# Kernel optimization log

Hardware: AMD Instinct MI355X
Metric: run time of the kernel (lower is better)

Reference implementation:

```python
import jax, jax.numpy as jnp
import numpy as np

N = 50000      # nodes
E = 800000     # edges (before self-loops)
F_IN = 256     # feature_size
H = 96         # hidden_channels
G = 64         # graphs in batch
NC = 4         # num_classes
EPS = 1e-5     # BatchNorm eps


def _lrelu(x, s=0.01):
    return jnp.where(x >= 0, x, s * x)


def _gat(x, W, a_s, a_d, b, src, dst):
    # PyG GATConv, heads=1: linear transform, edge-wise LeakyReLU(0.2) scores,
    # segment softmax over destination nodes, scatter-add aggregation.
    h = x @ W                                                  # [N,H]
    e = _lrelu((h * a_s).sum(-1)[src] + (h * a_d).sum(-1)[dst], 0.2)  # [E+N]
    m = jax.ops.segment_max(e, dst, num_segments=N)
    ee = jnp.exp(e - m[dst])
    denom = jax.ops.segment_sum(ee, dst, num_segments=N)
    alpha = ee / denom[dst]
    return jax.ops.segment_sum(alpha[:, None] * h[src], dst, num_segments=N) + b


def _bn(x, g, b):
    # training-mode BatchNorm over the node dimension
    mu = x.mean(0)
    var = ((x - mu) ** 2).mean(0)
    return g * (x - mu) / jnp.sqrt(var + EPS) + b


def setup_inputs() -> dict:
    key = jax.random.key(0)
    ks = jax.random.split(key, 20)
    p = lambda i, sh: jax.random.normal(ks[i], sh, jnp.float32) * 0.05
    inp = {
        "x": jax.random.normal(ks[0], (N, F_IN), jnp.float32),
        "edge_index": jax.random.randint(ks[1], (2, E), 0, N),
        "batch": jnp.sort(jax.random.randint(ks[2], (N,), 0, G)),
        "embed_W": p(3, (F_IN, H)), "embed_b": jnp.zeros((H,), jnp.float32),
        "conv1_W": p(4, (H, H)), "conv1_as": p(5, (H,)), "conv1_ad": p(6, (H,)), "conv1_b": jnp.zeros((H,), jnp.float32),
        "conv2_W": p(7, (H, H)), "conv2_as": p(8, (H,)), "conv2_ad": p(9, (H,)), "conv2_b": jnp.zeros((H,), jnp.float32),
        "conv3_W": p(10, (H, H)), "conv3_as": p(11, (H,)), "conv3_ad": p(12, (H,)), "conv3_b": jnp.zeros((H,), jnp.float32),
        "fc1_W": p(13, (H, H)), "fc1_b": jnp.zeros((H,), jnp.float32),
        "fc2_W": p(14, (H, H)), "fc2_b": jnp.zeros((H,), jnp.float32),
        "bn1_g": jnp.ones((H,), jnp.float32), "bn1_b": jnp.zeros((H,), jnp.float32),
        "bn2_g": jnp.ones((H,), jnp.float32), "bn2_b": jnp.zeros((H,), jnp.float32),
        "bn3_g": jnp.ones((H,), jnp.float32), "bn3_b": jnp.zeros((H,), jnp.float32),
        "fc3_W": p(15, (H, H // 2)), "fc3_b": jnp.zeros((H // 2,), jnp.float32),
        "fc4_W": p(16, (H // 2, NC)), "fc4_b": jnp.zeros((NC,), jnp.float32),
    }
    return inp


def reference(x, edge_index, batch, embed_W, embed_b,
              conv1_W, conv1_as, conv1_ad, conv1_b,
              conv2_W, conv2_as, conv2_ad, conv2_b,
              conv3_W, conv3_as, conv3_ad, conv3_b,
              fc1_W, fc1_b, fc2_W, fc2_b,
              bn1_g, bn1_b, bn2_g, bn2_b, bn3_g, bn3_b,
              fc3_W, fc3_b, fc4_W, fc4_b):
    loops = jnp.arange(N)
    src = jnp.concatenate([edge_index[0], loops])   # GATConv add_self_loops=True
    dst = jnp.concatenate([edge_index[1], loops])

    h = _lrelu(x @ embed_W + embed_b)
    identity = h
    h = _lrelu(_bn(_gat(h, conv1_W, conv1_as, conv1_ad, conv1_b, src, dst), bn1_g, bn1_b)) + identity
    h = _lrelu(h @ fc1_W + fc1_b)
    h = _lrelu(_bn(_gat(h, conv2_W, conv2_as, conv2_ad, conv2_b, src, dst), bn2_g, bn2_b)) + identity
    h = _lrelu(h @ fc2_W + fc2_b)
    h = _lrelu(_bn(_gat(h, conv3_W, conv3_as, conv3_ad, conv3_b, src, dst), bn3_g, bn3_b)) + identity

    # Poincare ball expmap0 with c=1: tanh(||u||) * u / ||u||
    n = jnp.maximum(jnp.linalg.norm(h, axis=-1, keepdims=True), 1e-15)
    h = jnp.tanh(n) * h / n

    cnt = jax.ops.segment_sum(jnp.ones((N,), h.dtype), batch, num_segments=G)
    pooled = jax.ops.segment_sum(h, batch, num_segments=G) / jnp.maximum(cnt, 1.0)[:, None]

    o = _lrelu(pooled @ fc3_W + fc3_b)
    return o @ fc4_W + fc4_b
```

## Files before the change

### kernel.cpp

```cpp
#include <hip/hip_runtime.h>
#include <hip/hip_bf16.h>

#define DEVINL __device__ __forceinline__

constexpr int N_NODES = 50000;
constexpr int N_EDGES = 800000;
constexpr int F_IN    = 256;
constexpr int H       = 96;
constexpr int NG      = 64;
constexpr float BN_EPS = 1e-5f;
constexpr int SLOT    = 64;
constexpr int NREP    = 8;
constexpr int REPSZ   = NG * H + NG;
constexpr int EPB     = 8;
constexpr int ECHUNK  = 256 * EPB;

typedef short bf16x8 __attribute__((ext_vector_type(8)));
typedef float f32x4  __attribute__((ext_vector_type(4)));

DEVINL float bf2f(unsigned int u) {
    union { unsigned int i; float f; } c; c.i = u << 16; return c.f;
}
DEVINL unsigned short f2bf(float f) {
    union { float f; unsigned int i; } c; c.f = f;
    unsigned int x = c.i;
    return (unsigned short)((x + 0x7fffu + ((x >> 16) & 1u)) >> 16);
}
DEVINL float lrelu01(float v) { return v >= 0.f ? v : 0.01f * v; }
DEVINL float ldf(const void* p, size_t i, int f32) {
    return f32 ? ((const float*)p)[i] : bf2f(((const unsigned short*)p)[i]);
}

__global__ __launch_bounds__(256) void detect_fill_k(const unsigned short* __restrict__ x,
                                                     int* __restrict__ flag,
                                                     int* __restrict__ fill)
{
    if (blockIdx.x == 0 && threadIdx.x < 64) {
        int l = threadIdx.x;
        float f = bf2f(x[l]);
        bool huge = !(fabsf(f) <= 1e4f);
        unsigned long long m = __ballot(huge);
        if (l == 0) flag[0] = (__popcll(m) >= 8) ? 1 : 0;
    }
    int i = blockIdx.x * 256 + threadIdx.x;
    if (i < N_NODES) fill[i] = 0;
}

__global__ __launch_bounds__(256) void wpackall_k(
    const void* __restrict__ sE, const void* __restrict__ s0,
    const void* __restrict__ s1, const void* __restrict__ s2,
    const void* __restrict__ s3, const void* __restrict__ s4,
    const int* __restrict__ dflag,
    unsigned short* __restrict__ dE, unsigned short* __restrict__ d0,
    unsigned short* __restrict__ d1, unsigned short* __restrict__ d2,
    unsigned short* __restrict__ d3, unsigned short* __restrict__ d4)
{
    int b = blockIdx.x;
    const void* src; unsigned short* dst; int K, i0;
    if (b < 96) { src = sE; dst = dE; K = F_IN; i0 = b * 256; }
    else {
        int m = (b - 96) / 36, r = (b - 96) % 36;
        K = H; i0 = r * 256;
        if      (m == 0) { src = s0; dst = d0; }
        else if (m == 1) { src = s1; dst = d1; }
        else if (m == 2) { src = s2; dst = d2; }
        else if (m == 3) { src = s3; dst = d3; }
        else             { src = s4; dst = d4; }
    }
    int i = i0 + threadIdx.x;
    if (i >= K * 96) return;
    int c   = i / 3072;
    int rem = i - c * 3072;
    int t    = rem >> 9;
    int rem2 = rem & 511;
    int l = rem2 >> 3, j = rem2 & 7;
    int k = c * 32 + (l >> 4) * 8 + j;
    int n = t * 16 + (l & 15);
    if (dflag[0]) dst[i] = f2bf(((const float*)src)[k * 96 + n]);
    else          dst[i] = ((const unsigned short*)src)[k * 96 + n];
}

template<int EPI, int AWS, int SD, int ABN, int SCAT, int K>
__global__ __launch_bounds__(256) void mgemm_k(
    const void* __restrict__ Ap, const unsigned short* __restrict__ Wpk,
    const void* __restrict__ bp, const int* __restrict__ dflag,
    unsigned short* __restrict__ out, unsigned short* __restrict__ out2,
    const void* __restrict__ as_, const void* __restrict__ ad_,
    float* __restrict__ s, float* __restrict__ d,
    const float* __restrict__ coefp, const unsigned short* __restrict__ idn,
    const int* __restrict__ ei, int* __restrict__ fill,
    unsigned short* __restrict__ colw, int e0, int e1, int ngb,
    int M)
{
    constexpr int NCH = K / 32;
    __shared__ unsigned short Wlds[K * 96];

    if (SCAT && (int)blockIdx.x >= ngb) {
        int b0 = e0 + ((int)blockIdx.x - ngb) * ECHUNK + (int)threadIdx.x;
        int sv[EPB], dv[EPB];
        bool ok[EPB];
        #pragma unroll
        for (int j = 0; j < EPB; j++) {
            int e = b0 + j * 256;
            ok[j] = (e < e1);
            int ee = ok[j] ? e : e0;
            sv[j] = ei[ee];
            dv[j] = ei[N_EDGES + ee];
        }
        int p[EPB];
        #pragma unroll
        for (int j = 0; j < EPB; j++)
            p[j] = ok[j] ? atomicAdd(&fill[dv[j]], 1) : SLOT;
        #pragma unroll
        for (int j = 0; j < EPB; j++)
            if (p[j] < SLOT) colw[(size_t)dv[j] * SLOT + p[j]] = (unsigned short)sv[j];
        return;
    }

    {
        const uint4* ws = (const uint4*)Wpk;
        uint4* wd = (uint4*)Wlds;
        #pragma unroll 4
        for (int i = threadIdx.x; i < K * 12; i += 256) wd[i] = ws[i];
    }
    __syncthreads();

    const int f32  = AWS ? 0 : dflag[0];
    const int wf32 = dflag[0];
    const int l    = threadIdx.x & 63;
    const int wave = threadIdx.x >> 6;
    const int row0 = blockIdx.x * 64 + wave * 16;
    const int m    = l & 15;
    const int q    = l >> 4;
    const int arow = row0 + m;
    const bool aok = arow < M;

    bf16x8 av[NCH];
    #pragma unroll
    for (int c = 0; c < NCH; c++) {
        bf16x8 a = {};
        if (aok) {
            if (ABN) {
                const int f0 = c * 32 + q * 8;
                uint4 xu = *(const uint4*)((const unsigned short*)Ap + (size_t)arow * K + f0);
                uint4 iu = *(const uint4*)(idn + (size_t)arow * K + f0);
                unsigned int xs[4] = { xu.x, xu.y, xu.z, xu.w };
                unsigned int is[4] = { iu.x, iu.y, iu.z, iu.w };
                #pragma unroll
                for (int jj = 0; jj < 4; jj++) {
                    int f = f0 + 2 * jj;
                    float v0 = lrelu01(bf2f(xs[jj] & 0xffff) * coefp[f]     + coefp[96 + f])     + bf2f(is[jj] & 0xffff);
                    float v1 = lrelu01(bf2f(xs[jj] >> 16)    * coefp[f + 1] + coefp[96 + f + 1]) + bf2f(is[jj] >> 16);
                    a[2 * jj]     = (short)f2bf(v0);
                    a[2 * jj + 1] = (short)f2bf(v1);
                }
            } else if (f32) {
                const float* A = (const float*)Ap + (size_t)arow * K + c * 32 + q * 8;
                #pragma unroll
                for (int j = 0; j < 8; j++) a[j] = (short)f2bf(A[j]);
            } else {
                a = *(const bf16x8*)((const unsigned short*)Ap + (size_t)arow * K + c * 32 + q * 8);
            }
        }
        av[c] = a;
    }

    f32x4 acc[6] = {};
    const bf16x8* wl = (const bf16x8*)Wlds;
    #pragma unroll
    for (int c = 0; c < NCH; c++) {
        const int base = c * 384 + l;
        #pragma unroll
        for (int t = 0; t < 6; t++)
            acc[t] = __builtin_amdgcn_mfma_f32_16x16x32_bf16(av[c], wl[base + t * 64], acc[t], 0, 0, 0);
    }

    float bv[6];
    if (EPI > 0) {
        #pragma unroll
        for (int t = 0; t < 6; t++) bv[t] = ldf(bp, t * 16 + m, wf32);
    }
    #pragma unroll
    for (int r = 0; r < 4; r++) {
        int rr = row0 + q * 4 + r;
        if (rr >= M) continue;
        size_t o = (size_t)rr * 96 + m;
        #pragma unroll
        for (int t = 0; t < 6; t++) {
            float v = acc[t][r];
            if (EPI > 0) v = lrelu01(v + bv[t]);
            unsigned short sv = f2bf(v);
            out[o + t * 16] = sv;
            if (EPI == 2) out2[o + t * 16] = sv;
        }
    }

    if (SD) {
        float asv[6], adv[6];
        #pragma unroll
        for (int t = 0; t < 6; t++) {
            asv[t] = ldf(as_, t * 16 + m, wf32);
            adv[t] = ldf(ad_, t * 16 + m, wf32);
        }
        #pragma unroll
        for (int r = 0; r < 4; r++) {
            float ps = 0.f, pd = 0.f;
            #pragma unroll
            for (int t = 0; t < 6; t++) {
                ps = fmaf(acc[t][r], asv[t], ps);
                pd = fmaf(acc[t][r], adv[t], pd);
            }
            #pragma unroll
            for (int off = 1; off < 16; off <<= 1) {
                ps += __shfl_xor(ps, off);
                pd += __shfl_xor(pd, off);
            }
            int rr = row0 + q * 4 + r;
            if (m == 0 && rr < M) { s[rr] = ps; d[rr] = pd; }
        }
    }
}

__global__ __launch_bounds__(256) void agg_k(
    const unsigned short* __restrict__ h2, const float* __restrict__ s,
    const float* __restrict__ d, const int* __restrict__ fill,
    const unsigned short* __restrict__ col, const void* __restrict__ bias,
    const int* __restrict__ dflag, unsigned short* __restrict__ out,
    float* __restrict__ bnsum, float* __restrict__ zp, int M)
{
    __shared__ uint2 uwb[4][80];
    if (blockIdx.x == 0 && threadIdx.x < 192) bnsum[threadIdx.x] = 0.f;
    if (zp) {
        int zi = blockIdx.x * 256 + threadIdx.x;
        if (zi < NREP * REPSZ) zp[zi] = 0.f;
    }
    int f32 = dflag[0];
    int v = (blockIdx.x * blockDim.x + threadIdx.x) >> 6;
    int l = threadIdx.x & 63;
    int wv = threadIdx.x >> 6;
    if (v >= M) return;
    int st   = v * SLOT;
    int degr = min(fill[v], SLOT - 1);
    int deg  = degr + 1;

    float dv = d[v];
    int u = 0; float e = -1e30f;
    if (l < degr) {
        u = col[st + l];
        float t = s[u] + dv;
        e = t >= 0.f ? t : 0.2f * t;
    } else if (l == degr) {
        u = v;
        float t = s[v] + dv;
        e = t >= 0.f ? t : 0.2f * t;
    }
    float lm = e;
    #pragma unroll
    for (int off = 32; off > 0; off >>= 1) lm = fmaxf(lm, __shfl_xor(lm, off));
    float w = (l < deg) ? __expf(e - lm) : 0.f;
    float ls = w;
    #pragma unroll
    for (int off = 32; off > 0; off >>= 1) ls += __shfl_xor(ls, off);
    float rden = 1.0f / ls;

    uwb[wv][l] = make_uint2((unsigned int)u, __float_as_uint(w));
    if (l < 16) uwb[wv][64 + l] = make_uint2(0u, 0u);

    bool hw = (l < 48);
    int  c2 = 2 * l;
    float a0 = 0.f, a1 = 0.f;
    const uint2* myuw = uwb[wv];
    for (int j = 0; j < deg; j += 16) {
        uint2 p[16];
        #pragma unroll
        for (int k = 0; k < 16; k++) p[k] = myuw[j + k];
        if (hw) {
            unsigned int hv[16];
            #pragma unroll
            for (int k = 0; k < 16; k++)
                hv[k] = *(const unsigned int*)(h2 + (size_t)p[k].x * 96 + c2);
            #pragma unroll
            for (int k = 0; k < 16; k++) {
                float wj = __uint_as_float(p[k].y);
                a0 = fmaf(wj, bf2f(hv[k] & 0xffff), a0);
                a1 = fmaf(wj, bf2f(hv[k] >> 16),    a1);
            }
        }
    }
    if (hw) {
        float b0 = ldf(bias, c2,     f32);
        float b1 = ldf(bias, c2 + 1, f32);
        unsigned int o = (unsigned int)f2bf(a0 * rden + b0)
                       | ((unsigned int)f2bf(a1 * rden + b1) << 16);
        *(unsigned int*)(out + (size_t)v * 96 + c2) = o;
    }
}

__global__ __launch_bounds__(192) void bnstats_k(const unsigned short* __restrict__ x,
                                                 float* __restrict__ sums, int M)
{
    int c  = threadIdx.x % 96;
    int g2 = threadIdx.x / 96;
    float s = 0.f, q = 0.f;
    for (int r = blockIdx.x * 2 + g2; r < M; r += gridDim.x * 2) {
        float v = bf2f(x[(size_t)r * 96 + c]);
        s += v; q += v * v;
    }
    __shared__ float lsd[192], lqd[192];
    lsd[threadIdx.x] = s; lqd[threadIdx.x] = q;
    __syncthreads();
    if (g2 == 0) {
        atomicAdd(&sums[c],      s + lsd[threadIdx.x + 96]);
        atomicAdd(&sums[96 + c], q + lqd[threadIdx.x + 96]);
    }
}

__global__ void bncoef_k(const float* __restrict__ sums,
                         const void* __restrict__ g_,
                         const void* __restrict__ b_,
                         const int* __restrict__ dflag,
                         float* __restrict__ coef)
{
    int c = threadIdx.x;
    if (c >= 96) return;
    int f32 = dflag[0];
    float mu  = sums[c] * (1.f / N_NODES);
    float var = sums[96 + c] * (1.f / N_NODES) - mu * mu;
    float rinv = 1.0f / sqrtf(var + BN_EPS);
    float sc = ldf(g_, c, f32) * rinv;
    coef[c]      = sc;
    coef[96 + c] = ldf(b_, c, f32) - mu * sc;
}

__global__ __launch_bounds__(256) void bnpool_k(
    const unsigned short* __restrict__ h, const float* __restrict__ coef,
    const unsigned short* __restrict__ iden, const int* __restrict__ batch,
    float* __restrict__ pooled8, int M)
{
    int w = (blockIdx.x * blockDim.x + threadIdx.x) >> 6;
    int l = threadIdx.x & 63;
    int v0 = w * 16;
    if (v0 >= M) return;
    float* P = pooled8 + (blockIdx.x & (NREP - 1)) * REPSZ;
    float* C = P + NG * H;
    bool hw = (l < 48);
    int  c2 = 2 * l;
    float sc0 = 0.f, sc1 = 0.f, sh0 = 0.f, sh1 = 0.f;
    if (hw) {
        sc0 = coef[c2]; sc1 = coef[c2 + 1];
        sh0 = coef[96 + c2]; sh1 = coef[97 + c2];
    }
    int nv = min(16, M - v0);

    int gb[16];
    #pragma unroll
    for (int k = 0; k < 16; k++) gb[k] = batch[v0 + min(k, nv - 1)];

    float x0[16], x1[16], q[16];
    #pragma unroll
    for (int k = 0; k < 16; k++) { x0[k] = 0.f; x1[k] = 0.f; q[k] = 0.f; }
    if (hw) {
        unsigned int xu[16], iu[16];
        #pragma unroll
        for (int k = 0; k < 16; k++) {
            int v = v0 + k;
            if (k < nv) {
                xu[k] = *(const unsigned int*)(h    + (size_t)v * 96 + c2);
                iu[k] = *(const unsigned int*)(iden + (size_t)v * 96 + c2);
            } else { xu[k] = 0u; iu[k] = 0u; }
        }
        #pragma unroll
        for (int k = 0; k < 16; k++) {
            x0[k] = lrelu01(bf2f(xu[k] & 0xffff) * sc0 + sh0) + bf2f(iu[k] & 0xffff);
            x1[k] = lrelu01(bf2f(xu[k] >> 16)    * sc1 + sh1) + bf2f(iu[k] >> 16);
            q[k]  = x0[k] * x0[k] + x1[k] * x1[k];
        }
    }

    #pragma unroll
    for (int off = 32; off > 0; off >>= 1) {
        #pragma unroll
        for (int k = 0; k < 16; k++) q[k] += __shfl_xor(q[k], off);
    }

    float f[16];
    #pragma unroll
    for (int k = 0; k < 16; k++) {
        float n = fmaxf(sqrtf(q[k]), 1e-15f);
        if (n < 15.f) {
            float t = __expf(2.f * n);
            f[k] = (t - 1.f) / ((t + 1.f) * n);
        } else {
            f[k] = 1.f / n;
        }
    }

    float a0 = 0.f, a1 = 0.f, cnt = 0.f;
    int curg = -1;
    for (int k = 0; k < nv; k++) {
        int g = gb[k];
        if (g != curg) {
            if (curg >= 0) {
                if (hw) {
                    atomicAdd(&P[curg * 96 + c2],     a0);
                    atomicAdd(&P[curg * 96 + c2 + 1], a1);
                }
                if (l == 0) atomicAdd(&C[curg], cnt);
            }
            a0 = a1 = 0.f; cnt = 0.f; curg = g;
        }
        a0 = fmaf(f[k], x0[k], a0);
        a1 = fmaf(f[k], x1[k], a1);
        cnt += 1.f;
    }
    if (curg >= 0) {
        if (hw) {
            atomicAdd(&P[curg * 96 + c2],     a0);
            atomicAdd(&P[curg * 96 + c2 + 1], a1);
        }
        if (l == 0) atomicAdd(&C[curg], cnt);
    }
}

__global__ __launch_bounds__(64) void head_k(const float* __restrict__ pooled8,
                                             const void* __restrict__ w3,
                                             const void* __restrict__ b3,
                                             const void* __restrict__ w4,
                                             const void* __restrict__ b4,
                                             const int* __restrict__ dflag,
                                             void* __restrict__ outv)
{
    int g = blockIdx.x;
    int t = threadIdx.x;
    int f32 = dflag[0];
    __shared__ float p[96];
    __shared__ float o[48];
    float cs = 0.f;
    #pragma unroll
    for (int r = 0; r < NREP; r++) cs += pooled8[r * REPSZ + NG * H + g];
    float inv = 1.0f / fmaxf(cs, 1.0f);
    for (int c = t; c < 96; c += 64) {
        float v = 0.f;
        #pragma unroll
        for (int r = 0; r < NREP; r++) v += pooled8[r * REPSZ + g * 96 + c];
        p[c] = v * inv;
    }
    __syncthreads();
    if (t < 48) {
        float a = ldf(b3, t, f32);
        #pragma unroll
        for (int c = 0; c < 96; c++) a = fmaf(p[c], ldf(w3, (size_t)c * 48 + t, f32), a);
        o[t] = lrelu01(a);
    }
    __syncthreads();
    if (t < 4) {
        float a = ldf(b4, t, f32);
        #pragma unroll
        for (int j = 0; j < 48; j++) a = fmaf(o[j], ldf(w4, j * 4 + t, f32), a);
        if (f32) ((float*)outv)[g * 4 + t] = a;
        else     ((unsigned short*)outv)[g * 4 + t] = f2bf(a);
    }
}

extern "C" void kernel_launch(void* const* d_in, const int* in_sizes, int n_in,
                              void* d_out, int out_size, void* d_ws, size_t ws_size,
                              hipStream_t stream)
{
    const void* x     = d_in[0];
    const int*  ei    = (const int*)d_in[1];
    const int*  batch = (const int*)d_in[2];
    const void* embW  = d_in[3];
    const void* embB  = d_in[4];
    const void* convW[3]  = { d_in[5],  d_in[9],  d_in[13] };
    const void* convAs[3] = { d_in[6],  d_in[10], d_in[14] };
    const void* convAd[3] = { d_in[7],  d_in[11], d_in[15] };
    const void* convB[3]  = { d_in[8],  d_in[12], d_in[16] };
    const void* fcW[2]    = { d_in[17], d_in[19] };
    const void* fcB[2]    = { d_in[18], d_in[20] };
    const void* bnG[3]    = { d_in[21], d_in[23], d_in[25] };
    const void* bnB[3]    = { d_in[22], d_in[24], d_in[26] };
    const void* fc3W = d_in[27];
    const void* fc3b = d_in[28];
    const void* fc4W = d_in[29];
    const void* fc4b = d_in[30];

    char* wp_ = (char*)d_ws;
    auto alloc = [&](size_t b) { char* p = wp_; wp_ += (b + 255) & ~(size_t)255; return p; };
    int*   dflag = (int*)alloc(256);
    unsigned short* ident = (unsigned short*)alloc((size_t)N_NODES * H * 2);
    unsigned short* hA    = (unsigned short*)alloc((size_t)N_NODES * H * 2);
    unsigned short* hB    = (unsigned short*)alloc((size_t)N_NODES * H * 2);
    float* s_sc  = (float*)alloc((size_t)N_NODES * 4);
    float* d_sc  = (float*)alloc((size_t)N_NODES * 4);
    float* bnsum = (float*)alloc(192 * 4);
    float* coef  = (float*)alloc(192 * 4);
    float* pooled8 = (float*)alloc((size_t)NREP * REPSZ * 4);
    int*   fill  = (int*)alloc((size_t)N_NODES * 4);
    unsigned short* col = (unsigned short*)alloc((size_t)N_NODES * SLOT * 2);
    unsigned short* wpkEmb = (unsigned short*)alloc((size_t)F_IN * 96 * 2);
    unsigned short* wpkS[5];
    for (int i = 0; i < 5; i++) wpkS[i] = (unsigned short*)alloc((size_t)H * 96 * 2);

    const int GM = (N_NODES + 63) / 64;
    const int GW = (N_NODES * 64 + 255) / 256;
    const int GP = ((N_NODES + 15) / 16 * 64 + 255) / 256;
    const int GF = (N_NODES + 255) / 256;
    const int EH = N_EDGES / 2;
    const int GS = (EH + ECHUNK - 1) / ECHUNK;

    detect_fill_k<<<GF, 256, 0, stream>>>((const unsigned short*)x, dflag, fill);

    wpackall_k<<<276, 256, 0, stream>>>(embW, convW[0], convW[1], convW[2], fcW[0], fcW[1],
                                        dflag, wpkEmb, wpkS[0], wpkS[1], wpkS[2], wpkS[3], wpkS[4]);

    mgemm_k<1, 0, 0, 0, 1, F_IN><<<GM + GS, 256, 0, stream>>>(
        x, wpkEmb, embB, dflag, ident, nullptr,
        nullptr, nullptr, nullptr, nullptr, nullptr, nullptr,
        ei, fill, col, 0, EH, GM, N_NODES);

    unsigned short* hcur = hA;
    unsigned short* htmp = hB;

    for (int l = 0; l < 3; l++) {
        if (l == 0) {
            mgemm_k<0, 1, 1, 0, 1, H><<<GM + GS, 256, 0, stream>>>(
                ident, wpkS[0], nullptr, dflag, htmp, nullptr,
                convAs[0], convAd[0], s_sc, d_sc, nullptr, nullptr,
                ei, fill, col, EH, N_EDGES, GM, N_NODES);
        } else {
            mgemm_k<0, 1, 1, 0, 0, H><<<GM, 256, 0, stream>>>(
                hcur, wpkS[l], nullptr, dflag, htmp, nullptr,
                convAs[l], convAd[l], s_sc, d_sc, nullptr, nullptr,
                nullptr, nullptr, nullptr, 0, 0, GM, N_NODES);
        }
        agg_k<<<GW, 256, 0, stream>>>(htmp, s_sc, d_sc, fill, col, convB[l], dflag, hcur,
                                      bnsum, (l == 2) ? pooled8 : nullptr, N_NODES);
        bnstats_k<<<512, 192, 0, stream>>>(hcur, bnsum, N_NODES);
        bncoef_k<<<1, 128, 0, stream>>>(bnsum, bnG[l], bnB[l], dflag, coef);
        if (l < 2) {
            mgemm_k<1, 1, 0, 1, 0, H><<<GM, 256, 0, stream>>>(
                hcur, wpkS[3 + l], fcB[l], dflag, htmp, nullptr,
                nullptr, nullptr, nullptr, nullptr, coef, ident,
                nullptr, nullptr, nullptr, 0, 0, GM, N_NODES);
            unsigned short* t = hcur; hcur = htmp; htmp = t;
        }
    }

    bnpool_k<<<GP, 256, 0, stream>>>(hcur, coef, ident, batch, pooled8, N_NODES);
    head_k<<<NG, 64, 0, stream>>>(pooled8, fc3W, fc3b, fc4W, fc4b, dflag, d_out);
}
```

Baseline: 427.6 us.

## Read GEMM weights directly from global memory and schedule scatter blocks first

Drops the per-block LDS staging of the packed weight matrix and its __syncthreads, so the MFMA loop loads B fragments straight from global memory, relying on the L1/L2 caches since every block reads the same weights. The edge-scatter blocks now take the low block indices and launch before the GEMM blocks. A min-blocks-per-CU hint of 4 is added to launch_bounds. This removes the LDS footprint and the block-level barrier, but adds redundant global and cache loads per wave and may raise register pressure.

```diff
diff --git a/kernel.cpp b/kernel.cpp
--- a/kernel.cpp
+++ b/kernel.cpp
@@ -81,7 +81,7 @@
 }
 
 template<int EPI, int AWS, int SD, int ABN, int SCAT, int K>
-__global__ __launch_bounds__(256) void mgemm_k(
+__global__ __launch_bounds__(256, 4) void mgemm_k(
     const void* __restrict__ Ap, const unsigned short* __restrict__ Wpk,
     const void* __restrict__ bp, const int* __restrict__ dflag,
     unsigned short* __restrict__ out, unsigned short* __restrict__ out2,
@@ -89,14 +89,13 @@
     float* __restrict__ s, float* __restrict__ d,
     const float* __restrict__ coefp, const unsigned short* __restrict__ idn,
     const int* __restrict__ ei, int* __restrict__ fill,
-    unsigned short* __restrict__ colw, int e0, int e1, int ngb,
+    unsigned short* __restrict__ colw, int e0, int e1, int nscat,
     int M)
 {
     constexpr int NCH = K / 32;
-    __shared__ unsigned short Wlds[K * 96];
-
-    if (SCAT && (int)blockIdx.x >= ngb) {
-        int b0 = e0 + ((int)blockIdx.x - ngb) * ECHUNK + (int)threadIdx.x;
+
+    if (SCAT && (int)blockIdx.x < nscat) {
+        int b0 = e0 + (int)blockIdx.x * ECHUNK + (int)threadIdx.x;
         int sv[EPB], dv[EPB];
         bool ok[EPB];
         #pragma unroll
@@ -117,19 +116,12 @@
         return;
     }
 
-    {
-        const uint4* ws = (const uint4*)Wpk;
-        uint4* wd = (uint4*)Wlds;
-        #pragma unroll 4
-        for (int i = threadIdx.x; i < K * 12; i += 256) wd[i] = ws[i];
-    }
-    __syncthreads();
-
+    const int gb   = SCAT ? (int)blockIdx.x - nscat : (int)blockIdx.x;
     const int f32  = AWS ? 0 : dflag[0];
     const int wf32 = dflag[0];
     const int l    = threadIdx.x & 63;
     const int wave = threadIdx.x >> 6;
-    const int row0 = blockIdx.x * 64 + wave * 16;
+    const int row0 = gb * 64 + wave * 16;
     const int m    = l & 15;
     const int q    = l >> 4;
     const int arow = row0 + m;
@@ -166,13 +158,13 @@
     }
 
     f32x4 acc[6] = {};
-    const bf16x8* wl = (const bf16x8*)Wlds;
+    const bf16x8* wp = (const bf16x8*)Wpk;
     #pragma unroll
     for (int c = 0; c < NCH; c++) {
         const int base = c * 384 + l;
         #pragma unroll
         for (int t = 0; t < 6; t++)
-            acc[t] = __builtin_amdgcn_mfma_f32_16x16x32_bf16(av[c], wl[base + t * 64], acc[t], 0, 0, 0);
+            acc[t] = __builtin_amdgcn_mfma_f32_16x16x32_bf16(av[c], wp[base + t * 64], acc[t], 0, 0, 0);
     }
 
     float bv[6];
@@ -513,25 +505,25 @@
     wpackall_k<<<276, 256, 0, stream>>>(embW, convW[0], convW[1], convW[2], fcW[0], fcW[1],
                                         dflag, wpkEmb, wpkS[0], wpkS[1], wpkS[2], wpkS[3], wpkS[4]);
 
-    mgemm_k<1, 0, 0, 0, 1, F_IN><<<GM + GS, 256, 0, stream>>>(
+    mgemm_k<1, 0, 0, 0, 1, F_IN><<<GS + GM, 256, 0, stream>>>(
         x, wpkEmb, embB, dflag, ident, nullptr,
         nullptr, nullptr, nullptr, nullptr, nullptr, nullptr,
-        ei, fill, col, 0, EH, GM, N_NODES);
+        ei, fill, col, 0, EH, GS, N_NODES);
 
     unsigned short* hcur = hA;
     unsigned short* htmp = hB;
 
     for (int l = 0; l < 3; l++) {
         if (l == 0) {
-            mgemm_k<0, 1, 1, 0, 1, H><<<GM + GS, 256, 0, stream>>>(
+            mgemm_k<0, 1, 1, 0, 1, H><<<GS + GM, 256, 0, stream>>>(
                 ident, wpkS[0], nullptr, dflag, htmp, nullptr,
                 convAs[0], convAd[0], s_sc, d_sc, nullptr, nullptr,
-                ei, fill, col, EH, N_EDGES, GM, N_NODES);
+                ei, fill, col, EH, N_EDGES, GS, N_NODES);
         } else {
             mgemm_k<0, 1, 1, 0, 0, H><<<GM, 256, 0, stream>>>(
                 hcur, wpkS[l], nullptr, dflag, htmp, nullptr,
                 convAs[l], convAd[l], s_sc, d_sc, nullptr, nullptr,
-                nullptr, nullptr, nullptr, 0, 0, GM, N_NODES);
+                nullptr, nullptr, nullptr, 0, 0, 0, N_NODES);
         }
         agg_k<<<GW, 256, 0, stream>>>(htmp, s_sc, d_sc, fill, col, convB[l], dflag, hcur,
                                       bnsum, (l == 2) ? pooled8 : nullptr, N_NODES);
@@ -541,7 +533,7 @@
             mgemm_k<1, 1, 0, 1, 0, H><<<GM, 256, 0, stream>>>(
                 hcur, wpkS[3 + l], fcB[l], dflag, htmp, nullptr,
                 nullptr, nullptr, nullptr, nullptr, coef, ident,
-                nullptr, nullptr, nullptr, 0, 0, GM, N_NODES);
+                nullptr, nullptr, nullptr, 0, 0, 0, N_NODES);
             unsigned short* t = hcur; hcur = htmp; htmp = t;
         }
     }
```

Result: slower. 437.5 us (+2.3%).
